# Kernel optimization log

Measured on AMD Instinct MI355X. Metric: run time of the kernel, lower is better.

Reference implementation:

```python
import jax, jax.numpy as jnp
import numpy as np

NUM_SEGMENTS = 128  # number of graphs (index.max()+1)


def setup_inputs() -> dict:
    key = jax.random.key(0)
    k1, k2, k3 = jax.random.split(key, 3)
    N, F, T, S, B = 200000, 3, 32, 32, NUM_SEGMENTS
    x = jax.random.normal(k1, (N, F), dtype=jnp.float32)
    v = jax.random.normal(k2, (F, T), dtype=jnp.float32)
    # lin exactly as in the module: linspace(-r, r, bump_steps).view(-1,1,1)
    lin = jnp.linspace(-1.1, 1.1, S, dtype=jnp.float32).reshape(S, 1, 1)
    index = jnp.sort(jax.random.randint(k3, (N,), 0, B, dtype=jnp.int64))
    return {"x": x, "index": index, "v": v, "lin": lin, "scale": 500}


def reference(x, index, v, lin, scale):
    # nh: node heights [N, T]
    nh = x @ v
    # ecc: [S, N, T] broadcasted sigmoid bump
    ecc = jax.nn.sigmoid(scale * (lin - nh))
    # scatter-add over nodes into per-graph bins, then movedim(0,1):
    # segment_sum over leading axis after transposing to [N, S, T]
    # gives [B, S, T] directly (== index_add over dim 1 then movedim).
    out = jax.ops.segment_sum(jnp.transpose(ecc, (1, 0, 2)), index,
                              num_segments=NUM_SEGMENTS)
    return out
```

## Files before the change

### kernel.cpp

```cpp
#include <hip/hip_runtime.h>

#define NSEG 128
#define SSTEPS 32
#define TDIM 32
#define NG 8
#define DROWS 35
#define SPB 8
#define CSTR (DROWS * TDIM)
#define UNR 4

__global__ __launch_bounds__(256) void ect_kernel(
    const float* __restrict__ x,
    const int*   __restrict__ idx,
    const float* __restrict__ v,
    const float* __restrict__ lin,
    const int*   __restrict__ scale_p,
    float*       __restrict__ out,
    int N)
{
    __shared__ float d[NG][DROWS][TDIM];
    __shared__ int s_bounds[2];

    const int tid = threadIdx.x;
    const unsigned bx = blockIdx.x;
    const int b = bx >> 3;
    const int j = bx & (SPB - 1);

    if (tid < 64) {
        const int L = tid & 31;
        const int h = tid >> 5;
        const int target = b + h;
        const int g0 = (int)(((long long)target * N) >> 7);

        const int hi_last = idx[N - 1];
        int p1 = g0 - 1024 + 64 * L;
        int pc1 = min(max(p1, 0), N - 1);
        int val32 = idx[pc1];
        const bool is64 = (hi_last == 0);
        int val = is64 ? idx[2 * pc1] : val32;

        bool pred1 = (p1 < 0) ? true : ((p1 >= N) ? false : (val < target));
        unsigned long long m1 = __ballot(pred1);
        unsigned hm1 = (unsigned)(m1 >> (h * 32));

        if (hm1 == 0u || hm1 == 0xFFFFFFFFu) {
            if (L == 0) {
                int lo = 0, hi = N;
                while (lo < hi) {
                    int mid = (lo + hi) >> 1;
                    int vv = is64 ? idx[2 * mid] : idx[mid];
                    if (vv < target) lo = mid + 1; else hi = mid;
                }
                s_bounds[h] = lo;
            }
        } else {
            const int A = g0 - 1024 + 64 * (31 - __builtin_clz(hm1));
            int p2 = A + 1 + 2 * L;
            int pc2 = min(max(p2, 0), N - 1);
            int v2 = is64 ? idx[2 * pc2] : idx[pc2];
            bool pred2 = (p2 < 0) ? true : ((p2 >= N) ? false : (v2 < target));
            unsigned long long m2 = __ballot(pred2);
            unsigned hm2 = (unsigned)(m2 >> (h * 32));
            const int B = hm2 ? (A + 1 + 2 * (31 - __builtin_clz(hm2))) : A;
            int p3 = B + 1;
            int pc3 = min(p3, N - 1);
            int v3 = is64 ? idx[2 * pc3] : idx[pc3];
            bool pred3 = (p3 >= N) ? false : (v3 < target);
            if (L == 0) s_bounds[h] = pred3 ? (B + 2) : (B + 1);
        }
    }
    {
        float4* dz = (float4*)d;
        for (int i = tid; i < NG * CSTR / 4; i += 256)
            dz[i] = make_float4(0.f, 0.f, 0.f, 0.f);
    }

    const float lin0 = lin[0];
    const float step = lin[1] - lin0;
    const float inv_step = 1.0f / step;
    const float negl0 = -lin0 * inv_step;
    const float scale = (float)scale_p[0];
    const float zstep = scale * step;

    const int t = tid & 31;
    const int g = tid >> 5;
    const float v0 = v[t], v1 = v[TDIM + t], v2 = v[2 * TDIM + t];
    float* dg = &d[g][0][t];

    __syncthreads();

    const int start = s_bounds[0], end = s_bounds[1];
    const int cnt_n = end - start;
    const int chunk = (cnt_n + SPB - 1) / SPB;
    const int k0 = start + j * chunk;
    const int k1 = min(k0 + chunk, end);

    float cnt = 0.f;

    auto process = [&](float x0, float x1, float x2) {
        const float nh = fmaf(x0, v0, fmaf(x1, v1, x2 * v2));

        float u = fmaf(nh, inv_step, negl0);
        u = fminf(fmaxf(u, -2.0f), 34.0f);
        const float rf = rintf(u);

        if (rf >= 32.0f) return;
        if (rf <= -2.0f) { cnt += 1.0f; return; }

        const float E = __expf((rf - u) * zstep);
        const float a = E * __builtin_amdgcn_rcpf(1.0f + E);

        const int row = (int)rf + 2;
        float* p = dg + row * 32;
        const float a0 = p[0];
        const float a1 = p[32];
        p[0]  = a0 + a;
        p[32] = a1 + (1.0f - a);
    };

    {
        int k = k0 + g;
        const int nit = (k < k1) ? ((k1 - k) + NG - 1) / NG : 0;
        const int nb = nit / UNR;

        float cx[UNR][3];
        if (nb > 0) {
            #pragma unroll
            for (int i = 0; i < UNR; ++i) {
                const int kk = k + i * NG;
                cx[i][0] = x[kk * 3 + 0];
                cx[i][1] = x[kk * 3 + 1];
                cx[i][2] = x[kk * 3 + 2];
            }
        }
        for (int bi = 0; bi < nb; ++bi) {
            const int knext = k + UNR * NG;
            const bool more = (bi + 1 < nb);
            float nx[UNR][3];
            #pragma unroll
            for (int i = 0; i < UNR; ++i) {
                const int kk = more ? (knext + i * NG) : k;
                nx[i][0] = x[kk * 3 + 0];
                nx[i][1] = x[kk * 3 + 1];
                nx[i][2] = x[kk * 3 + 2];
            }
            #pragma unroll
            for (int i = 0; i < UNR; ++i)
                process(cx[i][0], cx[i][1], cx[i][2]);
            #pragma unroll
            for (int i = 0; i < UNR; ++i) {
                cx[i][0] = nx[i][0]; cx[i][1] = nx[i][1]; cx[i][2] = nx[i][2];
            }
            k = knext;
        }
        for (k = k0 + g + nb * UNR * NG; k < k1; k += NG)
            process(x[k * 3 + 0], x[k * 3 + 1], x[k * 3 + 2]);
    }
    dg[0] = cnt;
    __syncthreads();

    {
        float4* c0 = (float4*)d;
        for (int i = tid; i < CSTR / 4; i += 256) {
            float4 a = c0[i];
            #pragma unroll
            for (int gg = 1; gg < NG; ++gg) {
                const float4 bq = ((const float4*)((const float*)d + gg * CSTR))[i];
                a.x += bq.x; a.y += bq.y; a.z += bq.z; a.w += bq.w;
            }
            c0[i] = a;
        }
    }
    __syncthreads();

    if (tid < TDIM) {
        float* df = (float*)d;
        float run = df[tid] + df[32 + tid];
        #pragma unroll
        for (int s = 0; s < SSTEPS; ++s) {
            run += df[(s + 2) * 32 + tid];
            df[(s + 2) * 32 + tid] = run;
        }
    }
    __syncthreads();

    {
        const float* df = (const float*)d;
        float* ob = out + (size_t)b * (SSTEPS * TDIM);
        #pragma unroll
        for (int q = 0; q < 4; ++q)
            atomicAdd(&ob[q * 256 + tid], df[64 + q * 256 + tid]);
    }
}

extern "C" void kernel_launch(void* const* d_in, const int* in_sizes, int n_in,
                              void* d_out, int out_size, void* d_ws, size_t ws_size,
                              hipStream_t stream) {
    const float* x     = (const float*)d_in[0];
    const int*   index = (const int*)d_in[1];
    const float* v     = (const float*)d_in[2];
    const float* lin   = (const float*)d_in[3];
    const int*   scale = (const int*)d_in[4];
    float* out = (float*)d_out;
    const int N = in_sizes[0] / 3;

    hipMemsetAsync(d_out, 0, (size_t)out_size * sizeof(float), stream);
    ect_kernel<<<NSEG * SPB, 256, 0, stream>>>(x, index, v, lin, scale, out, N);
}
```

Baseline: 72.97 us.

## Stage node coordinates in LDS per group and parallelize prefix scan

Assigns each 32-thread group a contiguous node range, cooperatively loads 32 coordinate rows into shared memory and has threads read them as broadcasts instead of per-thread global loads. Overlaps shared-memory zeroing with the boundary search threads, and replaces the serial 32-step bin scan with a two-level parallel scan across all threads. Drops the explicit register prefetch pipeline and relies on wavefront lockstep for LDS staging correctness without barriers.

```diff
diff --git a/kernel.cpp b/kernel.cpp
--- a/kernel.cpp
+++ b/kernel.cpp
@@ -7,9 +7,9 @@
 #define DROWS 35
 #define SPB 8
 #define CSTR (DROWS * TDIM)
-#define UNR 4
-
-__global__ __launch_bounds__(256) void ect_kernel(
+#define THREADS 256
+
+__global__ __launch_bounds__(THREADS) void ect_kernel(
     const float* __restrict__ x,
     const int*   __restrict__ idx,
     const float* __restrict__ v,
@@ -19,6 +19,7 @@
     int N)
 {
     __shared__ float d[NG][DROWS][TDIM];
+    __shared__ float4 xs[NG][32];
     __shared__ int s_bounds[2];
 
     const int tid = threadIdx.x;
@@ -68,10 +69,9 @@
             bool pred3 = (p3 >= N) ? false : (v3 < target);
             if (L == 0) s_bounds[h] = pred3 ? (B + 2) : (B + 1);
         }
-    }
-    {
+    } else {
         float4* dz = (float4*)d;
-        for (int i = tid; i < NG * CSTR / 4; i += 256)
+        for (int i = tid - 64; i < NG * CSTR / 4; i += THREADS - 64)
             dz[i] = make_float4(0.f, 0.f, 0.f, 0.f);
     }
 
@@ -95,73 +95,51 @@
     const int k0 = start + j * chunk;
     const int k1 = min(k0 + chunk, end);
 
-    float cnt = 0.f;
-
-    auto process = [&](float x0, float x1, float x2) {
-        const float nh = fmaf(x0, v0, fmaf(x1, v1, x2 * v2));
-
-        float u = fmaf(nh, inv_step, negl0);
-        u = fminf(fmaxf(u, -2.0f), 34.0f);
-        const float rf = rintf(u);
-
-        if (rf >= 32.0f) return;
-        if (rf <= -2.0f) { cnt += 1.0f; return; }
-
-        const float E = __expf((rf - u) * zstep);
-        const float a = E * __builtin_amdgcn_rcpf(1.0f + E);
-
-        const int row = (int)rf + 2;
-        float* p = dg + row * 32;
-        const float a0 = p[0];
-        const float a1 = p[32];
-        p[0]  = a0 + a;
-        p[32] = a1 + (1.0f - a);
-    };
-
-    {
-        int k = k0 + g;
-        const int nit = (k < k1) ? ((k1 - k) + NG - 1) / NG : 0;
-        const int nb = nit / UNR;
-
-        float cx[UNR][3];
-        if (nb > 0) {
-            #pragma unroll
-            for (int i = 0; i < UNR; ++i) {
-                const int kk = k + i * NG;
-                cx[i][0] = x[kk * 3 + 0];
-                cx[i][1] = x[kk * 3 + 1];
-                cx[i][2] = x[kk * 3 + 2];
-            }
-        }
-        for (int bi = 0; bi < nb; ++bi) {
-            const int knext = k + UNR * NG;
-            const bool more = (bi + 1 < nb);
-            float nx[UNR][3];
-            #pragma unroll
-            for (int i = 0; i < UNR; ++i) {
-                const int kk = more ? (knext + i * NG) : k;
-                nx[i][0] = x[kk * 3 + 0];
-                nx[i][1] = x[kk * 3 + 1];
-                nx[i][2] = x[kk * 3 + 2];
-            }
-            #pragma unroll
-            for (int i = 0; i < UNR; ++i)
-                process(cx[i][0], cx[i][1], cx[i][2]);
-            #pragma unroll
-            for (int i = 0; i < UNR; ++i) {
-                cx[i][0] = nx[i][0]; cx[i][1] = nx[i][1]; cx[i][2] = nx[i][2];
-            }
-            k = knext;
-        }
-        for (k = k0 + g + nb * UNR * NG; k < k1; k += NG)
-            process(x[k * 3 + 0], x[k * 3 + 1], x[k * 3 + 2]);
-    }
-    dg[0] = cnt;
+    {
+        const int span = k1 - k0;
+        const int cg = (span > 0) ? ((span + NG - 1) >> 3) : 0;
+        const int kg0 = k0 + g * cg;
+        const int kg1 = min(kg0 + cg, k1);
+        float4* xsg = &xs[g][0];
+        float cnt = 0.f;
+
+        for (int kb = kg0; kb < kg1; kb += 32) {
+            const int nb = min(32, kg1 - kb);
+            if (t < nb) {
+                const float* xp = x + (size_t)(kb + t) * 3;
+                xsg[t] = make_float4(xp[0], xp[1], xp[2], 0.f);
+            }
+            float4 cur = xsg[0];
+            for (int r = 0; r < nb; ++r) {
+                const float4 nxt = xsg[min(r + 1, nb - 1)];
+
+                const float nh = fmaf(cur.x, v0, fmaf(cur.y, v1, cur.z * v2));
+                float u = fmaf(nh, inv_step, negl0);
+                u = fminf(fmaxf(u, -2.0f), 34.0f);
+                const float rf = rintf(u);
+                if (rf < 32.0f) {
+                    if (rf <= -2.0f) cnt += 1.0f;
+                    else {
+                        const float E = __expf((rf - u) * zstep);
+                        const float a = E * __builtin_amdgcn_rcpf(1.0f + E);
+                        const int row = (int)rf + 2;
+                        float* p = dg + row * 32;
+                        const float a0 = p[0];
+                        const float a1 = p[32];
+                        p[0]  = a0 + a;
+                        p[32] = a1 + (1.0f - a);
+                    }
+                }
+                cur = nxt;
+            }
+        }
+        dg[0] = cnt;
+    }
     __syncthreads();
 
     {
         float4* c0 = (float4*)d;
-        for (int i = tid; i < CSTR / 4; i += 256) {
+        for (int i = tid; i < CSTR / 4; i += THREADS) {
             float4 a = c0[i];
             #pragma unroll
             for (int gg = 1; gg < NG; ++gg) {
@@ -173,14 +151,28 @@
     }
     __syncthreads();
 
-    if (tid < TDIM) {
+    {
         float* df = (float*)d;
-        float run = df[tid] + df[32 + tid];
+        float* sums = (float*)xs;
+        const int rb = tid >> 5;
+        const int rowb = 2 + rb * 4;
+        float w0 = df[(rowb + 0) * 32 + t];
+        float w1 = df[(rowb + 1) * 32 + t];
+        float w2 = df[(rowb + 2) * 32 + t];
+        float w3 = df[(rowb + 3) * 32 + t];
+        w1 += w0; w2 += w1; w3 += w2;
+        sums[rb * 32 + t] = w3;
+        __syncthreads();
+        float off = df[t] + df[32 + t];
         #pragma unroll
-        for (int s = 0; s < SSTEPS; ++s) {
-            run += df[(s + 2) * 32 + tid];
-            df[(s + 2) * 32 + tid] = run;
-        }
+        for (int r = 0; r < 8; ++r) {
+            const float sv = sums[r * 32 + t];
+            off += (r < rb) ? sv : 0.f;
+        }
+        df[(rowb + 0) * 32 + t] = w0 + off;
+        df[(rowb + 1) * 32 + t] = w1 + off;
+        df[(rowb + 2) * 32 + t] = w2 + off;
+        df[(rowb + 3) * 32 + t] = w3 + off;
     }
     __syncthreads();
 
@@ -205,5 +197,5 @@
     const int N = in_sizes[0] / 3;
 
     hipMemsetAsync(d_out, 0, (size_t)out_size * sizeof(float), stream);
-    ect_kernel<<<NSEG * SPB, 256, 0, stream>>>(x, index, v, lin, scale, out, N);
+    ect_kernel<<<NSEG * SPB, THREADS, 0, stream>>>(x, index, v, lin, scale, out, N);
 }
```

Result: no change. 71.91 us (-1.5%).
